# Kernel optimization log

Hardware: AMD Instinct MI355X
Metric: run time of the kernel (lower is better)

Reference implementation:

```python
import jax, jax.numpy as jnp
import numpy as np
from jax import lax


def setup_inputs() -> dict:
    key = jax.random.key(0)
    k1, k2 = jax.random.split(key)
    x = jax.random.normal(k1, (32, 128, 64, 64), dtype=jnp.float32)
    # learned kernel, original shape (k, k, in_channels, out_channels)
    K = jax.random.normal(k2, (3, 3, 128, 256), dtype=jnp.float32) * 0.05
    return {"x": x, "K": K}


def reference(x, K):
    stride, padding = 1, 1
    kh = K.shape[0]
    C = K.shape[2]
    O = K.shape[3]
    H = x.shape[-1]
    P = H + 2 * padding
    out_size = (P - kh) // stride + 1
    # Original pairs x-patches flattened as (C, kh, kw) with K flattened
    # row-major as (kh, kw, C), matched purely by flat index. Equivalent to a
    # standard conv with the weight buffer reinterpreted as (C, kh, kw, O):
    W = K.reshape(-1, O).reshape(C, kh, kh, O).transpose(3, 0, 1, 2)  # (O,C,kh,kw)
    out = lax.conv_general_dilated(
        x, W,
        window_strides=(stride, stride),
        padding=[(padding, padding), (padding, padding)],
        dimension_numbers=("NCHW", "OIHW", "NCHW"),
    )  # (B, O, out_size, out_size)
    # Original loop uses range(0, P - kh, stride) (missing +1): when
    # (P - kh) % stride == 0 the last output row/col is never written (stays 0).
    n_filled = -(-(P - kh) // stride)  # ceil((P-kh)/stride), static
    if n_filled < out_size:
        out = out.at[:, :, n_filled:, :].set(0.0)
        out = out.at[:, :, :, n_filled:].set(0.0)
    return out
```

## Files before the change

kernel.cpp:

```cpp
#include <hip/hip_runtime.h>
#include <hip/hip_bf16.h>

typedef __attribute__((ext_vector_type(8))) short bf16x8;
typedef __attribute__((ext_vector_type(4))) float f32x4;

#define CIN   128
#define HW    64
#define OUTC  256

#define BP_OFF     33554432ULL
#define ZP_OFF     34144256ULL
#define WS_NEEDED  34148352ULL

#define SB  __builtin_amdgcn_s_barrier()
#define SCB __builtin_amdgcn_sched_barrier(0)
#define WAITV(N) asm volatile("s_waitcnt vmcnt(" #N ")" ::: "memory")
#define MFMA(a, b, c) __builtin_amdgcn_mfma_f32_16x16x32_bf16(a, b, c, 0, 0, 0)

__global__ __launch_bounds__(256) void conv_prep(const float* __restrict__ X,
                                                 const float* __restrict__ Kw,
                                                 __hip_bfloat16* __restrict__ Xt2,
                                                 __hip_bfloat16* __restrict__ Bp2,
                                                 __hip_bfloat16* __restrict__ zp) {
    const int blk = blockIdx.x;
    if (blk < 2048) {
        __shared__ __hip_bfloat16 L[64][136];
        const int b = blk >> 6;
        const int y = blk & 63;
        const int x = threadIdx.x & 63;
        const int c0 = (threadIdx.x >> 6) * 32;
        const float* src = X + (((long)(b * CIN + c0) * HW + y) * HW + x);
        #pragma unroll
        for (int j = 0; j < 32; j += 2) {
            float v0 = src[(long)j * (HW * HW)];
            float v1 = src[(long)(j + 1) * (HW * HW)];
            __hip_bfloat162 p;
            p.x = __float2bfloat16(v0);
            p.y = __float2bfloat16(v1);
            *reinterpret_cast<__hip_bfloat162*>(&L[x][c0 + j]) = p;
        }
        __syncthreads();
        const int xx = threadIdx.x >> 2;
        const int g  = threadIdx.x & 3;
        #pragma unroll
        for (int cc = 0; cc < 4; ++cc) {
            bf16x8 v = *reinterpret_cast<const bf16x8*>(&L[xx][cc * 32 + g * 8]);
            long dst = (((long)(b * 4 + cc) * 64 + y) * 64 + xx) * 32 + g * 8;
            *reinterpret_cast<bf16x8*>(&Xt2[dst]) = v;
        }
    } else if (blk < 2112) {
        for (int i = (blk - 2048) * 256 + threadIdx.x; i < 294912; i += 64 * 256) {
            int c32 = i & 31;
            int n   = (i >> 5) & 255;
            int cc  = (i >> 13) & 3;
            int ij  = i >> 15;
            int c   = cc * 32 + c32;
            Bp2[i] = __float2bfloat16(Kw[(c * 9 + ij) * 256 + n]);
        }
    } else {
        *reinterpret_cast<float4*>((char*)zp + threadIdx.x * 16) = float4{0.f, 0.f, 0.f, 0.f};
    }
}

__global__ __launch_bounds__(512, 2) void conv_igemm7(
    const __hip_bfloat16* __restrict__ Xt2,
    const __hip_bfloat16* __restrict__ Bp2,
    const __hip_bfloat16* __restrict__ zp,
    float* __restrict__ out)
{
    __shared__ __hip_bfloat16 As[4][256 * 32];
    __shared__ __hip_bfloat16 Bs[4][256 * 32];

    const int tid  = threadIdx.x;
    const int wv   = tid >> 6;
    const int lane = tid & 63;
    const int l16  = lane & 15;
    const int d16  = lane >> 4;
    const int wr   = wv >> 2;
    const int wc   = wv & 3;

    const int bid   = blockIdx.x;
    const int mtile = (bid & 7) * 64 + (bid >> 3);
    const int b  = mtile >> 4;
    const int y0 = (mtile & 15) * 4;

    const int srow = lane >> 2;
    const int sg   = lane & 3;

    f32x4 acc[8][4] = {};

    const int r0  = wv * 32 + srow;
    const int r1  = r0 + 16;
    const int G0  = (sg - (r0 >> 1)) & 3;
    const int G1  = (sg - (r1 >> 1)) & 3;
    const int xr0 = r0 & 63, xr1 = r1 & 63;
    const int yy0 = y0 + (r0 >> 6), yy1 = y0 + (r1 >> 6);
    const __hip_bfloat16* pA0 = Xt2 + (((long)b * 16384 + yy0 * 64 + xr0) * 32 + G0 * 8);
    const __hip_bfloat16* pA1 = Xt2 + (((long)b * 16384 + yy1 * 64 + xr1) * 32 + G1 * 8);
    const __hip_bfloat16* pB0 = Bp2 + ((long)r0 * 32 + G0 * 8);
    const __hip_bfloat16* pB1 = Bp2 + ((long)r1 * 32 + G1 * 8);
    const __hip_bfloat16* zp0 = zp + G0 * 8;
    const __hip_bfloat16* zp1 = zp + G1 * 8;
    const int ldsOff0 = (wv * 32) * 32;
    const int ldsOff1 = (wv * 32 + 16) * 32;

    auto stage = [&](int S) {
        const int ij = S >> 2;
        const int cc = S & 3;
        const int di = ij / 3 - 1;
        const int dj = ij % 3 - 1;
        const long offA = ((long)cc * 4096 + di * 64 + dj) * 32;
        const bool ok0 = ((unsigned)(xr0 + dj) < 64u) && ((unsigned)(yy0 + di) < 64u);
        const bool ok1 = ((unsigned)(xr1 + dj) < 64u) && ((unsigned)(yy1 + di) < 64u);
        const __hip_bfloat16* gA0 = ok0 ? pA0 + offA : zp0;
        const __hip_bfloat16* gA1 = ok1 ? pA1 + offA : zp1;
        __hip_bfloat16* ldsA = &As[S & 3][0];
        __builtin_amdgcn_global_load_lds(
            (const __attribute__((address_space(1))) void*)gA0,
            (__attribute__((address_space(3))) void*)(ldsA + ldsOff0), 16, 0, 0);
        __builtin_amdgcn_global_load_lds(
            (const __attribute__((address_space(1))) void*)gA1,
            (__attribute__((address_space(3))) void*)(ldsA + ldsOff1), 16, 0, 0);
        const long offB = (long)(ij * 4 + cc) * 8192;
        __hip_bfloat16* ldsB = &Bs[S & 3][0];
        __builtin_amdgcn_global_load_lds(
            (const __attribute__((address_space(1))) void*)(pB0 + offB),
            (__attribute__((address_space(3))) void*)(ldsB + ldsOff0), 16, 0, 0);
        __builtin_amdgcn_global_load_lds(
            (const __attribute__((address_space(1))) void*)(pB1 + offB),
            (__attribute__((address_space(3))) void*)(ldsB + ldsOff1), 16, 0, 0);
    };

    stage(0); stage(1); stage(2);
    WAITV(8);
    SCB; SB;

    #pragma unroll
    for (int H = 0; H < 36; ++H) {
        const int RB = H & 3;
        bf16x8 Af[8], Bf[4];
        #pragma unroll
        for (int mi = 0; mi < 8; ++mi) {
            const int m = wr * 128 + mi * 16 + l16;
            const int s = (d16 + (m >> 1)) & 3;
            Af[mi] = *reinterpret_cast<const bf16x8*>(&As[RB][m * 32 + s * 8]);
        }
        #pragma unroll
        for (int ni = 0; ni < 4; ++ni) {
            const int n = wc * 64 + ni * 16 + l16;
            const int s = (d16 + (n >> 1)) & 3;
            Bf[ni] = *reinterpret_cast<const bf16x8*>(&Bs[RB][n * 32 + s * 8]);
        }
        if (H < 33) stage(H + 3);
        if (H < 33)       WAITV(8);
        else if (H == 33) WAITV(4);
        else if (H == 34) WAITV(0);
        SCB; SB;
        __builtin_amdgcn_s_setprio(1);
        #pragma unroll
        for (int ni = 0; ni < 4; ++ni)
            #pragma unroll
            for (int mi = 0; mi < 8; ++mi)
                acc[mi][ni] = MFMA(Af[mi], Bf[ni], acc[mi][ni]);
        __builtin_amdgcn_s_setprio(0);
        SCB; SB;
    }

    #pragma unroll
    for (int mi = 0; mi < 8; ++mi) {
        const int m  = wr * 128 + mi * 16 + d16 * 4;
        const int x0 = m & 63;
        const int y  = y0 + (m >> 6);
        #pragma unroll
        for (int ni = 0; ni < 4; ++ni) {
            const int o = wc * 64 + ni * 16 + l16;
            float4 v;
            v.x = acc[mi][ni][0];
            v.y = acc[mi][ni][1];
            v.z = acc[mi][ni][2];
            v.w = acc[mi][ni][3];
            if (y == HW - 1) { v.x = v.y = v.z = v.w = 0.f; }
            if (x0 + 3 == HW - 1) v.w = 0.f;
            *reinterpret_cast<float4*>(
                out + ((long)(b * OUTC + o) * 4096 + y * 64 + x0)) = v;
        }
    }
}

__global__ __launch_bounds__(256) void conv_igemm_bf16(
    const float* __restrict__ X, const float* __restrict__ Kw, float* __restrict__ out) {
    __shared__ __hip_bfloat16 As[128][40];
    __shared__ __hip_bfloat16 Bs[128][40];
    const int tid = threadIdx.x, wave = tid >> 6, lane = tid & 63;
    const int l16 = lane & 15, d16 = lane >> 4;
    const int m_base = blockIdx.x * 128;
    const int b = m_base >> 12, y0 = (m_base & 4095) >> 6;
    const int n_base = blockIdx.y * 128;
    const int wm = (wave >> 1) * 64, wn = (wave & 1) * 64;
    f32x4 acc[4][4] = {};
    const int smm = tid & 127, ccb = tid >> 7;
    const int sx = smm & 63, syr = smm >> 6;
    for (int ij = 0; ij < 9; ++ij) {
        const int di = ij / 3 - 1, dj = ij % 3 - 1;
        const int xp = sx + dj, yp = y0 + syr + di;
        const bool ok = ((unsigned)xp < 64u) && ((unsigned)yp < 64u);
        const long xbase = (((long)b * CIN) * HW + yp) * HW + xp;
        for (int c0 = 0; c0 < CIN; c0 += 32) {
            for (int cc = ccb; cc < 32; cc += 2) {
                float v = ok ? X[xbase + (long)(c0 + cc) * 4096] : 0.f;
                As[smm][cc] = __float2bfloat16(v);
                Bs[smm][cc] = __float2bfloat16(Kw[((c0 + cc) * 9 + ij) * OUTC + n_base + smm]);
            }
            __syncthreads();
            bf16x8 afrag[4], bfrag[4];
            for (int mi = 0; mi < 4; ++mi)
                afrag[mi] = *reinterpret_cast<const bf16x8*>(&As[wm + mi * 16 + l16][d16 * 8]);
            for (int ni = 0; ni < 4; ++ni)
                bfrag[ni] = *reinterpret_cast<const bf16x8*>(&Bs[wn + ni * 16 + l16][d16 * 8]);
            for (int mi = 0; mi < 4; ++mi)
                for (int ni = 0; ni < 4; ++ni)
                    acc[mi][ni] = __builtin_amdgcn_mfma_f32_16x16x32_bf16(
                        afrag[mi], bfrag[ni], acc[mi][ni], 0, 0, 0);
            __syncthreads();
        }
    }
    for (int mi = 0; mi < 4; ++mi)
        for (int ni = 0; ni < 4; ++ni)
            for (int r = 0; r < 4; ++r) {
                const int mm = wm + mi * 16 + d16 * 4 + r;
                const int nn = wn + ni * 16 + l16;
                const int y = y0 + (mm >> 6), x = mm & 63, o = n_base + nn;
                float v = acc[mi][ni][r];
                if (y == 63 || x == 63) v = 0.f;
                out[(((long)b * OUTC + o) * HW + y) * HW + x] = v;
            }
}

extern "C" void kernel_launch(void* const* d_in, const int* in_sizes, int n_in,
                              void* d_out, int out_size, void* d_ws, size_t ws_size,
                              hipStream_t stream) {
    const float* X  = (const float*)d_in[0];
    const float* Kw = (const float*)d_in[1];
    float* out = (float*)d_out;

    if (ws_size >= WS_NEEDED) {
        char* ws = (char*)d_ws;
        __hip_bfloat16* Xt2 = (__hip_bfloat16*)ws;
        __hip_bfloat16* Bp2 = (__hip_bfloat16*)(ws + BP_OFF);
        __hip_bfloat16* zp  = (__hip_bfloat16*)(ws + ZP_OFF);
        conv_prep<<<dim3(2113), dim3(256), 0, stream>>>(X, Kw, Xt2, Bp2, zp);
        conv_igemm7<<<dim3(512), dim3(512), 0, stream>>>(Xt2, Bp2, zp, out);
    } else {
        conv_igemm_bf16<<<dim3(1024, 2), dim3(256), 0, stream>>>(X, Kw, out);
    }
}
```

Before: 105.3 us.

## Shrink GEMM block tile to 128x256 with 4 waves and 3-stage LDS ring

```diff
diff --git a/kernel.cpp b/kernel.cpp
--- a/kernel.cpp
+++ b/kernel.cpp
@@ -62,99 +62,98 @@
     }
 }
 
-__global__ __launch_bounds__(512, 2) void conv_igemm7(
+__global__ __launch_bounds__(256, 2) void conv_igemm8(
     const __hip_bfloat16* __restrict__ Xt2,
     const __hip_bfloat16* __restrict__ Bp2,
     const __hip_bfloat16* __restrict__ zp,
     float* __restrict__ out)
 {
-    __shared__ __hip_bfloat16 As[4][256 * 32];
-    __shared__ __hip_bfloat16 Bs[4][256 * 32];
+    __shared__ __hip_bfloat16 As[3][128 * 32];
+    __shared__ __hip_bfloat16 Bs[3][256 * 32];
 
     const int tid  = threadIdx.x;
     const int wv   = tid >> 6;
     const int lane = tid & 63;
     const int l16  = lane & 15;
     const int d16  = lane >> 4;
-    const int wr   = wv >> 2;
-    const int wc   = wv & 3;
 
     const int bid   = blockIdx.x;
-    const int mtile = (bid & 7) * 64 + (bid >> 3);
-    const int b  = mtile >> 4;
-    const int y0 = (mtile & 15) * 4;
+    const int mtile = (bid & 7) * 128 + (bid >> 3);
+    const int b  = mtile >> 5;
+    const int y0 = (mtile & 31) * 2;
 
     const int srow = lane >> 2;
     const int sg   = lane & 3;
 
     f32x4 acc[8][4] = {};
 
-    const int r0  = wv * 32 + srow;
-    const int r1  = r0 + 16;
-    const int G0  = (sg - (r0 >> 1)) & 3;
-    const int G1  = (sg - (r1 >> 1)) & 3;
-    const int xr0 = r0 & 63, xr1 = r1 & 63;
-    const int yy0 = y0 + (r0 >> 6), yy1 = y0 + (r1 >> 6);
-    const __hip_bfloat16* pA0 = Xt2 + (((long)b * 16384 + yy0 * 64 + xr0) * 32 + G0 * 8);
-    const __hip_bfloat16* pA1 = Xt2 + (((long)b * 16384 + yy1 * 64 + xr1) * 32 + G1 * 8);
-    const __hip_bfloat16* pB0 = Bp2 + ((long)r0 * 32 + G0 * 8);
-    const __hip_bfloat16* pB1 = Bp2 + ((long)r1 * 32 + G1 * 8);
-    const __hip_bfloat16* zp0 = zp + G0 * 8;
-    const __hip_bfloat16* zp1 = zp + G1 * 8;
-    const int ldsOff0 = (wv * 32) * 32;
-    const int ldsOff1 = (wv * 32 + 16) * 32;
+    const int G = (sg - (srow >> 1)) & 3;
+
+    const int rA0 = wv * 32 + srow;
+    const int rA1 = rA0 + 16;
+    const int xA0 = rA0 & 63, xA1 = rA1 & 63;
+    const int yA0 = y0 + (rA0 >> 6), yA1 = y0 + (rA1 >> 6);
+    const __hip_bfloat16* pA0 = Xt2 + (((long)b * 16384 + yA0 * 64 + xA0) * 32 + G * 8);
+    const __hip_bfloat16* pA1 = Xt2 + (((long)b * 16384 + yA1 * 64 + xA1) * 32 + G * 8);
+    const __hip_bfloat16* zpg = zp + G * 8;
+    const int rB0 = wv * 64 + srow;
+    const __hip_bfloat16* pB = Bp2 + ((long)rB0 * 32 + G * 8);
+    const int ldsA0 = (wv * 32) * 32;
+    const int ldsA1 = (wv * 32 + 16) * 32;
+    const int ldsB0 = (wv * 64) * 32;
 
     auto stage = [&](int S) {
         const int ij = S >> 2;
         const int cc = S & 3;
         const int di = ij / 3 - 1;
         const int dj = ij % 3 - 1;
+        const int rs = S % 3;
         const long offA = ((long)cc * 4096 + di * 64 + dj) * 32;
-        const bool ok0 = ((unsigned)(xr0 + dj) < 64u) && ((unsigned)(yy0 + di) < 64u);
-        const bool ok1 = ((unsigned)(xr1 + dj) < 64u) && ((unsigned)(yy1 + di) < 64u);
-        const __hip_bfloat16* gA0 = ok0 ? pA0 + offA : zp0;
-        const __hip_bfloat16* gA1 = ok1 ? pA1 + offA : zp1;
-        __hip_bfloat16* ldsA = &As[S & 3][0];
+        const bool ok0 = ((unsigned)(xA0 + dj) < 64u) && ((unsigned)(yA0 + di) < 64u);
+        const bool ok1 = ((unsigned)(xA1 + dj) < 64u) && ((unsigned)(yA1 + di) < 64u);
+        const __hip_bfloat16* gA0 = ok0 ? pA0 + offA : zpg;
+        const __hip_bfloat16* gA1 = ok1 ? pA1 + offA : zpg;
+        __hip_bfloat16* ldsA = &As[rs][0];
         __builtin_amdgcn_global_load_lds(
             (const __attribute__((address_space(1))) void*)gA0,
-            (__attribute__((address_space(3))) void*)(ldsA + ldsOff0), 16, 0, 0);
+            (__attribute__((address_space(3))) void*)(ldsA + ldsA0), 16, 0, 0);
         __builtin_amdgcn_global_load_lds(
             (const __attribute__((address_space(1))) void*)gA1,
-            (__attribute__((address_space(3))) void*)(ldsA + ldsOff1), 16, 0, 0);
+            (__attribute__((address_space(3))) void*)(ldsA + ldsA1), 16, 0, 0);
         const long offB = (long)(ij * 4 + cc) * 8192;
-        __hip_bfloat16* ldsB = &Bs[S & 3][0];
-        __builtin_amdgcn_global_load_lds(
-            (const __attribute__((address_space(1))) void*)(pB0 + offB),
-            (__attribute__((address_space(3))) void*)(ldsB + ldsOff0), 16, 0, 0);
-        __builtin_amdgcn_global_load_lds(
-            (const __attribute__((address_space(1))) void*)(pB1 + offB),
-            (__attribute__((address_space(3))) void*)(ldsB + ldsOff1), 16, 0, 0);
+        __hip_bfloat16* ldsB = &Bs[rs][0];
+        #pragma unroll
+        for (int l = 0; l < 4; ++l) {
+            __builtin_amdgcn_global_load_lds(
+                (const __attribute__((address_space(1))) void*)(pB + offB + l * 512),
+                (__attribute__((address_space(3))) void*)(ldsB + ldsB0 + l * 512), 16, 0, 0);
+        }
     };
 
-    stage(0); stage(1); stage(2);
-    WAITV(8);
+    stage(0); stage(1);
+    WAITV(6);
     SCB; SB;
 
     #pragma unroll
     for (int H = 0; H < 36; ++H) {
-        const int RB = H & 3;
+        const int RB = H % 3;
         bf16x8 Af[8], Bf[4];
         #pragma unroll
         for (int mi = 0; mi < 8; ++mi) {
-            const int m = wr * 128 + mi * 16 + l16;
+            const int m = mi * 16 + l16;
             const int s = (d16 + (m >> 1)) & 3;
             Af[mi] = *reinterpret_cast<const bf16x8*>(&As[RB][m * 32 + s * 8]);
         }
         #pragma unroll
         for (int ni = 0; ni < 4; ++ni) {
-            const int n = wc * 64 + ni * 16 + l16;
+            const int n = wv * 64 + ni * 16 + l16;
             const int s = (d16 + (n >> 1)) & 3;
             Bf[ni] = *reinterpret_cast<const bf16x8*>(&Bs[RB][n * 32 + s * 8]);
         }
-        if (H < 33) stage(H + 3);
-        if (H < 33)       WAITV(8);
-        else if (H == 33) WAITV(4);
-        else if (H == 34) WAITV(0);
+        if (H < 34) stage(H + 2);
+        if (H < 34)       WAITV(12);
+        else if (H == 34) WAITV(6);
+        else              WAITV(0);
         SCB; SB;
         __builtin_amdgcn_s_setprio(1);
         #pragma unroll
@@ -168,12 +167,12 @@
 
     #pragma unroll
     for (int mi = 0; mi < 8; ++mi) {
-        const int m  = wr * 128 + mi * 16 + d16 * 4;
+        const int m  = mi * 16 + d16 * 4;
         const int x0 = m & 63;
         const int y  = y0 + (m >> 6);
         #pragma unroll
         for (int ni = 0; ni < 4; ++ni) {
-            const int o = wc * 64 + ni * 16 + l16;
+            const int o = wv * 64 + ni * 16 + l16;
             float4 v;
             v.x = acc[mi][ni][0];
             v.y = acc[mi][ni][1];
@@ -249,7 +248,7 @@
         __hip_bfloat16* Bp2 = (__hip_bfloat16*)(ws + BP_OFF);
         __hip_bfloat16* zp  = (__hip_bfloat16*)(ws + ZP_OFF);
         conv_prep<<<dim3(2113), dim3(256), 0, stream>>>(X, Kw, Xt2, Bp2, zp);
-        conv_igemm7<<<dim3(512), dim3(512), 0, stream>>>(Xt2, Bp2, zp, out);
+        conv_igemm8<<<dim3(1024), dim3(256), 0, stream>>>(Xt2, Bp2, zp, out);
     } else {
         conv_igemm_bf16<<<dim3(1024, 2), dim3(256), 0, stream>>>(X, Kw, out);
     }
```

After: 106.8 us. Within noise of the previous version (+1.4%).
